# Kernel optimization log

Measured on AMD Instinct MI355X. Metric: run time of the kernel, lower is better.

The kernel has to match this reference:

```python
import jax, jax.numpy as jnp
import numpy as np

D = 512

def setup_inputs() -> dict:
    key = jax.random.key(0)
    k1, k2, k3, k4 = jax.random.split(key, 4)
    inputs = jax.random.normal(k1, (8, 2048, D), dtype=jnp.float32)
    # torch nn.Linear weights are [out, in]; y = x @ W.T
    Wk = jax.random.normal(k2, (D, D), dtype=jnp.float32) / np.sqrt(D)
    Wq = jax.random.normal(k3, (D, D), dtype=jnp.float32) / np.sqrt(D)
    Wv = jax.random.normal(k4, (D, D), dtype=jnp.float32) / np.sqrt(D)
    return {"inputs": inputs, "Wk": Wk, "Wq": Wq, "Wv": Wv}

def reference(inputs, Wk, Wq, Wv):
    # q/k/v: [B, S, D]
    q = jnp.einsum('bsd,ed->bse', inputs, Wq)
    k = jnp.einsum('bsd,ed->bse', inputs, Wk)
    v = jnp.einsum('bsd,ed->bse', inputs, Wv)
    scores = jnp.einsum('bqd,bkd->bqk', q, k) * 5.0  # note: scale is *5, not 1/sqrt(d)
    attn = jax.nn.softmax(scores, axis=-1)
    # dropout is identity in eval mode
    out = jnp.einsum('bqk,bkd->bqd', attn, v)
    return jnp.swapaxes(out, -2, -1)  # [B, D, S]
```

## Files before the change

kernel.cpp:

```cpp
#include <hip/hip_runtime.h>
#include <stdint.h>

typedef __attribute__((ext_vector_type(4))) float f32x4;
typedef __attribute__((ext_vector_type(8))) short short8;
typedef unsigned short u16;
typedef unsigned int u32;

#define DEV static __device__ __forceinline__

DEV u32 fbits(float f) { union { float f; u32 u; } v; v.f = f; return v.u; }
DEV float bits2f(u32 u) { union { u32 u; float f; } v; v.u = u; return v.f; }

DEV u16 f2bf_rne(float f) {
  u32 u = fbits(f);
  u32 r = u + 0x7fffu + ((u >> 16) & 1u);
  return (u16)(r >> 16);
}
DEV u16 f2bf_trunc(float f) { return (u16)(fbits(f) >> 16); }
DEV float bf2f(u16 h) { return bits2f(((u32)h) << 16); }

DEV void split2(float f, u16& h, u16& l) {
  h = f2bf_rne(f);
  float r = f - bf2f(h);
  l = f2bf_trunc(r);
}

DEV void gll16(const void* gsrc, char* ldsp) {
  __builtin_amdgcn_global_load_lds(
      (const __attribute__((address_space(1))) u32*)gsrc,
      (__attribute__((address_space(3))) u32*)ldsp,
      16, 0, 0);
}

DEV f32x4 mfma16(short8 a, short8 b, f32x4 c) {
  return __builtin_amdgcn_mfma_f32_16x16x32_bf16(a, b, c, 0, 0, 0);
}

template<int EPI>
__global__ __launch_bounds__(256, 1) void proj_gemm(
    const float* __restrict__ A, const float* __restrict__ Bm,
    u16* __restrict__ o0, u16* __restrict__ o1, float scale)
{
  extern __shared__ char smem[];
  const int tid = threadIdx.x;
  const int lane = tid & 63, wv = tid >> 6;
  const int wm = wv & 1, wn = wv >> 1;
  const int lm = lane & 15, lg = lane >> 4;
  const int n0 = blockIdx.x * 128, m0 = blockIdx.y * 128;

  f32x4 acc[4][4] = {};

  for (int k0 = 0; k0 < 512; k0 += 64) {
    __syncthreads();
    #pragma unroll
    for (int i = 0; i < 8; ++i) {
      int c = i * 256 + tid;
      int row = c >> 4, c4 = c & 15;
      f32x4 av = *(const f32x4*)(A + (size_t)(m0 + row) * 512 + (k0 + c4 * 4));
      f32x4 bv = *(const f32x4*)(Bm + (size_t)(n0 + row) * 512 + (k0 + c4 * 4));
      int base = row * 128 + ((((c4 >> 1) ^ (row & 7)) << 4) + (c4 & 1) * 8);
      u16 ah[4], al[4], bh[4], bl[4];
      #pragma unroll
      for (int j = 0; j < 4; ++j) { split2(av[j], ah[j], al[j]); split2(bv[j], bh[j], bl[j]); }
      *(ushort4*)(smem +         base) = make_ushort4(ah[0], ah[1], ah[2], ah[3]);
      *(ushort4*)(smem + 16384 + base) = make_ushort4(al[0], al[1], al[2], al[3]);
      *(ushort4*)(smem + 32768 + base) = make_ushort4(bh[0], bh[1], bh[2], bh[3]);
      *(ushort4*)(smem + 49152 + base) = make_ushort4(bl[0], bl[1], bl[2], bl[3]);
    }
    __syncthreads();
    #pragma unroll
    for (int ks = 0; ks < 2; ++ks) {
      short8 fah[4], fal[4], fbh[4], fbl[4];
      #pragma unroll
      for (int t = 0; t < 4; ++t) {
        int ar = wm * 64 + t * 16 + lm;
        int ac = (((ks * 4 + lg) ^ (ar & 7)) << 4);
        fah[t] = *(const short8*)(smem +         ar * 128 + ac);
        fal[t] = *(const short8*)(smem + 16384 + ar * 128 + ac);
        int br = wn * 64 + t * 16 + lm;
        int bc = (((ks * 4 + lg) ^ (br & 7)) << 4);
        fbh[t] = *(const short8*)(smem + 32768 + br * 128 + bc);
        fbl[t] = *(const short8*)(smem + 49152 + br * 128 + bc);
      }
      #pragma unroll
      for (int mt = 0; mt < 4; ++mt)
        #pragma unroll
        for (int nt = 0; nt < 4; ++nt) {
          acc[mt][nt] = mfma16(fah[mt], fbh[nt], acc[mt][nt]);
          acc[mt][nt] = mfma16(fah[mt], fbl[nt], acc[mt][nt]);
          acc[mt][nt] = mfma16(fal[mt], fbh[nt], acc[mt][nt]);
        }
    }
  }
  #pragma unroll
  for (int mt = 0; mt < 4; ++mt)
    #pragma unroll
    for (int nt = 0; nt < 4; ++nt)
      #pragma unroll
      for (int i = 0; i < 4; ++i) {
        float v = acc[mt][nt][i] * scale;
        int m = m0 + wm * 64 + mt * 16 + lg * 4 + i;
        int n = n0 + wn * 64 + nt * 16 + lm;
        if (EPI == 0) {
          u16 h, l; split2(v, h, l);
          o0[(size_t)m * 512 + n] = h;
          o1[(size_t)m * 512 + n] = l;
        } else {
          int r = n & 31;
          int cc = ((r >> 2) & 3) * 8 + ((r >> 4) << 2) + (r & 3);
          int n2 = (n & ~31) | cc;
          size_t addr = ((size_t)(n >> 11) << 20) | ((size_t)m << 11) | (size_t)(n2 & 2047);
          o0[addr] = f2bf_rne(v);
        }
      }
}

#define QH_OFF 0
#define QL_OFF 65536
#define STG0   131072
#define STG1   147456

DEV void stage_chunk(const u16* __restrict__ kh, const u16* __restrict__ kl,
                     const u16* __restrict__ vt, char* smem, int buf,
                     int b, int kt, int c, int tid) {
  char* dst = smem + (buf ? STG1 : STG0);
  if (c < 8) {
    const size_t kbase = (size_t)b * 2048 * 512 + (size_t)kt * 64 * 512 + c * 64;
    #pragma unroll
    for (int j = 0; j < 2; ++j) {
      int slot = j * 256 + tid;
      int r = slot >> 3, ch = slot & 7, sc = ch ^ (r & 7);
      size_t src = kbase + (size_t)r * 512 + sc * 8;
      gll16(kh + src, dst + slot * 16);
      gll16(kl + src, dst + 8192 + slot * 16);
    }
  } else {
    const int cv = c - 8;
    const size_t vbase = (size_t)b * 512 * 2048 + (size_t)(cv * 128) * 2048 + (size_t)kt * 64;
    #pragma unroll
    for (int j = 0; j < 4; ++j) {
      int slot = j * 256 + tid;
      int r = slot >> 3, ch = slot & 7, sc = ch ^ (r & 7);
      gll16(vt + vbase + (size_t)r * 2048 + sc * 8, dst + slot * 16);
    }
  }
}

__global__ __launch_bounds__(256, 1) void attn_fused(
    const u16* __restrict__ qh, const u16* __restrict__ ql,
    const u16* __restrict__ kh, const u16* __restrict__ kl,
    const u16* __restrict__ vt, float* __restrict__ out)
{
  extern __shared__ char smem[];
  const int tid = threadIdx.x;
  const int lane = tid & 63, wv = tid >> 6;
  const int lm = lane & 15, lg = lane >> 4;
  const int b = blockIdx.x, qt = blockIdx.y;

  {
    const size_t qbase = (size_t)(b * 2048 + qt * 64) * 512;
    #pragma unroll
    for (int it = 0; it < 16; ++it) {
      int slot = it * 256 + tid;
      int row = slot >> 6, ch = slot & 63;
      int sc = ch ^ (row & 7);
      size_t src = qbase + (size_t)row * 512 + sc * 8;
      gll16(qh + src, smem + QH_OFF + slot * 16);
      gll16(ql + src, smem + QL_OFF + slot * 16);
    }
  }
  stage_chunk(kh, kl, vt, smem, 0, b, 0, 0, tid);

  float m = -3e38f, l = 0.f;
  f32x4 oacc[32] = {};
  short8 pb0 = {}, pb1 = {};
  const int qrow = wv * 16 + lm;

  for (int kt = 0; kt < 32; ++kt) {
    f32x4 sacc[4] = {};
    #pragma unroll
    for (int c = 0; c < 12; ++c) {
      {
        int nk = kt, nc = c + 1;
        if (nc == 12) { nc = 0; nk = (kt + 1) & 31; }
        stage_chunk(kh, kl, vt, smem, (c + 1) & 1, b, nk, nc, tid);
      }
      if (c == 8) {
        float mx = fmaxf(fmaxf(fmaxf(sacc[0][0], sacc[0][1]), fmaxf(sacc[0][2], sacc[0][3])),
                         fmaxf(fmaxf(sacc[1][0], sacc[1][1]), fmaxf(sacc[1][2], sacc[1][3])));
        mx = fmaxf(mx, fmaxf(fmaxf(fmaxf(sacc[2][0], sacc[2][1]), fmaxf(sacc[2][2], sacc[2][3])),
                             fmaxf(fmaxf(sacc[3][0], sacc[3][1]), fmaxf(sacc[3][2], sacc[3][3]))));
        mx = fmaxf(mx, __shfl_xor(mx, 16, 64));
        mx = fmaxf(mx, __shfl_xor(mx, 32, 64));
        if (__any(mx > m)) {
          float mn = fmaxf(m, mx);
          float alpha = __expf(m - mn);
          m = mn;
          #pragma unroll
          for (int f = 0; f < 32; ++f) {
            oacc[f][0] *= alpha; oacc[f][1] *= alpha;
            oacc[f][2] *= alpha; oacc[f][3] *= alpha;
          }
          l *= alpha;
        }
        float sm = 0.f;
        #pragma unroll
        for (int t4 = 0; t4 < 4; ++t4)
          #pragma unroll
          for (int i = 0; i < 4; ++i) {
            float p = __expf(sacc[t4][i] - m);
            sacc[t4][i] = p;
            sm += p;
          }
        sm += __shfl_xor(sm, 16, 64);
        sm += __shfl_xor(sm, 32, 64);
        l += sm;
        #pragma unroll
        for (int j = 0; j < 4; ++j) {
          pb0[j]     = (short)f2bf_rne(sacc[0][j]);
          pb0[4 + j] = (short)f2bf_rne(sacc[1][j]);
          pb1[j]     = (short)f2bf_rne(sacc[2][j]);
          pb1[4 + j] = (short)f2bf_rne(sacc[3][j]);
        }
      }
      asm volatile("s_waitcnt vmcnt(4)" ::: "memory");
      __builtin_amdgcn_s_barrier();
      __builtin_amdgcn_sched_barrier(0);
      const char* bufp = smem + ((c & 1) ? STG1 : STG0);
      if (c < 8) {
        #pragma unroll
        for (int ks = 0; ks < 2; ++ks) {
          int qg = c * 8 + ks * 4 + lg;
          short8 bqh = *(const short8*)(smem + QH_OFF + qrow * 1024 + ((qg ^ (qrow & 7)) << 4));
          short8 bql = *(const short8*)(smem + QL_OFF + qrow * 1024 + ((qg ^ (qrow & 7)) << 4));
          #pragma unroll
          for (int t4 = 0; t4 < 4; ++t4) {
            int krow = t4 * 16 + lm;
            int kc = ((ks * 4 + lg) ^ (krow & 7)) << 4;
            short8 akh = *(const short8*)(bufp + krow * 128 + kc);
            short8 akl = *(const short8*)(bufp + 8192 + krow * 128 + kc);
            sacc[t4] = mfma16(akh, bqh, sacc[t4]);
            sacc[t4] = mfma16(akh, bql, sacc[t4]);
            sacc[t4] = mfma16(akl, bqh, sacc[t4]);
          }
        }
      } else {
        const int cv = c - 8;
        #pragma unroll
        for (int dt = 0; dt < 8; ++dt) {
          int vrow = dt * 16 + lm;
          short8 av0 = *(const short8*)(bufp + vrow * 128 + ((lg ^ (vrow & 7)) << 4));
          short8 av1 = *(const short8*)(bufp + vrow * 128 + (((4 + lg) ^ (vrow & 7)) << 4));
          f32x4 o = oacc[cv * 8 + dt];
          o = mfma16(av0, pb0, o);
          o = mfma16(av1, pb1, o);
          oacc[cv * 8 + dt] = o;
        }
      }
      __builtin_amdgcn_sched_barrier(0);
      __builtin_amdgcn_s_barrier();
    }
  }
  float linv = 1.0f / l;
  const int s = qt * 64 + wv * 16 + lm;
  float* ob = out + ((size_t)b << 20) + s;
  #pragma unroll
  for (int f = 0; f < 32; ++f)
    #pragma unroll
    for (int i = 0; i < 4; ++i) {
      int d = f * 16 + lg * 4 + i;
      ob[(size_t)d * 2048] = oacc[f][i] * linv;
    }
}

extern "C" void kernel_launch(void* const* d_in, const int* in_sizes, int n_in,
                              void* d_out, int out_size, void* d_ws, size_t ws_size,
                              hipStream_t stream) {
  (void)in_sizes; (void)n_in; (void)out_size; (void)ws_size;
  const float* x  = (const float*)d_in[0];
  const float* Wk = (const float*)d_in[1];
  const float* Wq = (const float*)d_in[2];
  const float* Wv = (const float*)d_in[3];
  float* out = (float*)d_out;

  const size_t SZ = (size_t)16384 * 512;
  u16* q_hi = (u16*)d_ws;
  u16* q_lo = q_hi + SZ;
  u16* k_hi = q_lo + SZ;
  u16* k_lo = k_hi + SZ;
  u16* v_t  = k_lo + SZ;

  (void)hipFuncSetAttribute(reinterpret_cast<const void*>(&proj_gemm<0>),
                            hipFuncAttributeMaxDynamicSharedMemorySize, 65536);
  (void)hipFuncSetAttribute(reinterpret_cast<const void*>(&proj_gemm<1>),
                            hipFuncAttributeMaxDynamicSharedMemorySize, 65536);
  (void)hipFuncSetAttribute(reinterpret_cast<const void*>(&attn_fused),
                            hipFuncAttributeMaxDynamicSharedMemorySize, 163840);

  dim3 blk(256);
  proj_gemm<0><<<dim3(4, 128), blk, 65536, stream>>>(x, Wq, q_hi, q_lo, 5.0f);
  proj_gemm<0><<<dim3(4, 128), blk, 65536, stream>>>(x, Wk, k_hi, k_lo, 1.0f);
  proj_gemm<1><<<dim3(128, 4), blk, 65536, stream>>>(Wv, x, v_t, nullptr, 1.0f);
  attn_fused<<<dim3(8, 32), blk, 163840, stream>>>(q_hi, q_lo, k_hi, k_lo, v_t, out);
}
```

Before: 337.0 us.

## Switch attention to fp16 split precision with fp8 residual term and restructured pipeline

Replaces the bf16 hi/lo three-MFMA score computation with fp16 hi/lo products for Q and an fp8 MFMA for the scaled K residual term. Q fragments are now read directly from global memory rather than staged in LDS. P is passed through LDS so that each wave owns a slice of the head dimension for PV, and the V projection moves to a single fp16 GEMM. The aim is fewer and cheaper MFMAs plus less LDS traffic, at the cost of more barriers, extra staging stages, and accuracy risk from fp16/fp8 rounding.

New measurement: 514.1 us. 52.5% more time.

```diff
diff --git a/kernel.cpp b/kernel.cpp
--- a/kernel.cpp
+++ b/kernel.cpp
@@ -1,10 +1,13 @@
 #include <hip/hip_runtime.h>
 #include <stdint.h>
+#include <math.h>
 
 typedef __attribute__((ext_vector_type(4))) float f32x4;
 typedef __attribute__((ext_vector_type(8))) short short8;
+typedef __attribute__((ext_vector_type(8))) _Float16 half8;
 typedef unsigned short u16;
 typedef unsigned int u32;
+typedef unsigned char u8;
 
 #define DEV static __device__ __forceinline__
 
@@ -18,11 +21,38 @@
 }
 DEV u16 f2bf_trunc(float f) { return (u16)(fbits(f) >> 16); }
 DEV float bf2f(u16 h) { return bits2f(((u32)h) << 16); }
-
 DEV void split2(float f, u16& h, u16& l) {
   h = f2bf_rne(f);
   float r = f - bf2f(h);
   l = f2bf_trunc(r);
+}
+
+DEV u16 f2h(float f) { union { _Float16 h; u16 u; } v; v.h = (_Float16)f; return v.u; }
+DEV float h2f(u16 u) { union { u16 u; _Float16 h; } v; v.u = u; return (float)v.h; }
+DEV half8 as_h8(short8 s) { union { short8 s; half8 h; } u; u.s = s; return u.h; }
+DEV uint2 pk4h(f32x4 v) {
+  uint2 w;
+  w.x = (u32)f2h(v[0]) | ((u32)f2h(v[1]) << 16);
+  w.y = (u32)f2h(v[2]) | ((u32)f2h(v[3]) << 16);
+  return w;
+}
+
+DEV u8 f32_to_e4m3(float f) {
+  u32 sb = (fbits(f) >> 24) & 0x80u;
+  float a = fabsf(f);
+  if (!(a >= 0.001953125f)) return (u8)sb;
+  if (a > 448.f) return (u8)(sb | 0x7e);
+  int e; float mant = frexpf(a, &e);
+  int E = e + 6;
+  if (E <= 0) {
+    int mi = (int)(a * 512.f + 0.5f);
+    if (mi > 7) return (u8)(sb | 0x08);
+    return (u8)(sb | mi);
+  }
+  int mi = (int)((mant * 2.f - 1.f) * 8.f + 0.5f);
+  if (mi == 8) { mi = 0; ++E; }
+  if (E > 15 || (E == 15 && mi > 6)) return (u8)(sb | 0x7e);
+  return (u8)(sb | (E << 3) | mi);
 }
 
 DEV void gll16(const void* gsrc, char* ldsp) {
@@ -35,11 +65,18 @@
 DEV f32x4 mfma16(short8 a, short8 b, f32x4 c) {
   return __builtin_amdgcn_mfma_f32_16x16x32_bf16(a, b, c, 0, 0, 0);
 }
-
-template<int EPI>
-__global__ __launch_bounds__(256, 1) void proj_gemm(
+DEV f32x4 mfmah(half8 a, half8 b, f32x4 c) {
+  return __builtin_amdgcn_mfma_f32_16x16x32_f16(a, b, c, 0, 0, 0);
+}
+DEV f32x4 mfma8(long a, long b, f32x4 c) {
+  return __builtin_amdgcn_mfma_f32_16x16x32_fp8_fp8(a, b, c, 0, 0, 0);
+}
+
+template<int MODE>
+__global__ __launch_bounds__(256, 1) void proj_qk(
     const float* __restrict__ A, const float* __restrict__ Bm,
-    u16* __restrict__ o0, u16* __restrict__ o1, float scale)
+    u16* __restrict__ o0, u16* __restrict__ o1, u8* __restrict__ o2,
+    float scale)
 {
   extern __shared__ char smem[];
   const int tid = threadIdx.x;
@@ -101,107 +138,195 @@
         float v = acc[mt][nt][i] * scale;
         int m = m0 + wm * 64 + mt * 16 + lg * 4 + i;
         int n = n0 + wn * 64 + nt * 16 + lm;
-        if (EPI == 0) {
-          u16 h, l; split2(v, h, l);
-          o0[(size_t)m * 512 + n] = h;
-          o1[(size_t)m * 512 + n] = l;
+        size_t idx = (size_t)m * 512 + n;
+        u16 h = f2h(v);
+        float res = v - h2f(h);
+        o0[idx] = h;
+        if (MODE == 0) {
+          o1[idx] = f2h(res);
+          o2[idx] = f32_to_e4m3(h2f(h));
         } else {
-          int r = n & 31;
-          int cc = ((r >> 2) & 3) * 8 + ((r >> 4) << 2) + (r & 3);
-          int n2 = (n & ~31) | cc;
-          size_t addr = ((size_t)(n >> 11) << 20) | ((size_t)m << 11) | (size_t)(n2 & 2047);
-          o0[addr] = f2bf_rne(v);
-        }
-      }
-}
-
-#define QH_OFF 0
-#define QL_OFF 65536
-#define STG0   131072
-#define STG1   147456
-
-DEV void stage_chunk(const u16* __restrict__ kh, const u16* __restrict__ kl,
-                     const u16* __restrict__ vt, char* smem, int buf,
-                     int b, int kt, int c, int tid) {
-  char* dst = smem + (buf ? STG1 : STG0);
-  if (c < 8) {
-    const size_t kbase = (size_t)b * 2048 * 512 + (size_t)kt * 64 * 512 + c * 64;
-    #pragma unroll
-    for (int j = 0; j < 2; ++j) {
-      int slot = j * 256 + tid;
-      int r = slot >> 3, ch = slot & 7, sc = ch ^ (r & 7);
-      size_t src = kbase + (size_t)r * 512 + sc * 8;
-      gll16(kh + src, dst + slot * 16);
-      gll16(kl + src, dst + 8192 + slot * 16);
-    }
-  } else {
-    const int cv = c - 8;
-    const size_t vbase = (size_t)b * 512 * 2048 + (size_t)(cv * 128) * 2048 + (size_t)kt * 64;
-    #pragma unroll
-    for (int j = 0; j < 4; ++j) {
-      int slot = j * 256 + tid;
-      int r = slot >> 3, ch = slot & 7, sc = ch ^ (r & 7);
-      gll16(vt + vbase + (size_t)r * 2048 + sc * 8, dst + slot * 16);
-    }
+          o2[idx] = f32_to_e4m3(res * 4096.f);
+        }
+      }
+}
+
+__global__ __launch_bounds__(256, 1) void proj_v(
+    const float* __restrict__ A, const float* __restrict__ Bm,
+    u16* __restrict__ o0)
+{
+  extern __shared__ char smem[];
+  const int tid = threadIdx.x;
+  const int lane = tid & 63, wv = tid >> 6;
+  const int wm = wv & 1, wn = wv >> 1;
+  const int lm = lane & 15, lg = lane >> 4;
+  const int n0 = blockIdx.x * 128, m0 = blockIdx.y * 128;
+
+  f32x4 acc[4][4] = {};
+
+  for (int k0 = 0; k0 < 512; k0 += 64) {
+    __syncthreads();
+    #pragma unroll
+    for (int i = 0; i < 8; ++i) {
+      int c = i * 256 + tid;
+      int row = c >> 4, c4 = c & 15;
+      f32x4 av = *(const f32x4*)(A + (size_t)(m0 + row) * 512 + (k0 + c4 * 4));
+      f32x4 bv = *(const f32x4*)(Bm + (size_t)(n0 + row) * 512 + (k0 + c4 * 4));
+      int base = row * 128 + ((c4 ^ (2 * (row & 7))) << 3);
+      *(uint2*)(smem +         base) = pk4h(av);
+      *(uint2*)(smem + 16384 + base) = pk4h(bv);
+    }
+    __syncthreads();
+    #pragma unroll
+    for (int ks = 0; ks < 2; ++ks) {
+      half8 fa[4], fb[4];
+      #pragma unroll
+      for (int t = 0; t < 4; ++t) {
+        int ar = wm * 64 + t * 16 + lm;
+        fa[t] = as_h8(*(const short8*)(smem + ar * 128 + (((ks * 4 + lg) ^ (ar & 7)) << 4)));
+        int br = wn * 64 + t * 16 + lm;
+        fb[t] = as_h8(*(const short8*)(smem + 16384 + br * 128 + (((ks * 4 + lg) ^ (br & 7)) << 4)));
+      }
+      #pragma unroll
+      for (int mt = 0; mt < 4; ++mt)
+        #pragma unroll
+        for (int nt = 0; nt < 4; ++nt)
+          acc[mt][nt] = mfmah(fa[mt], fb[nt], acc[mt][nt]);
+    }
+  }
+  #pragma unroll
+  for (int mt = 0; mt < 4; ++mt)
+    #pragma unroll
+    for (int nt = 0; nt < 4; ++nt)
+      #pragma unroll
+      for (int i = 0; i < 4; ++i) {
+        int m = m0 + wm * 64 + mt * 16 + lg * 4 + i;
+        int n = n0 + wn * 64 + nt * 16 + lm;
+        size_t addr = ((size_t)(n >> 11) << 20) | ((size_t)m << 11) | (size_t)(n & 2047);
+        o0[addr] = f2h(acc[mt][nt][i]);
+      }
+}
+
+#define KHB(i)  ((i) * 40960)
+#define KLB(i)  ((i) * 40960 + 32768)
+#define VBUF(i) (81920 + (i) * 16384)
+#define PB      114688
+#define AB      122880
+#define ALDS    123392
+
+DEV void stageK(const u16* __restrict__ khp, const u8* __restrict__ klp,
+                char* smem, int b, int kt, int c, int tid) {
+  char* dh = smem + KHB(c & 1);
+  char* dl = smem + KLB(c & 1);
+  const size_t rbase = (size_t)(b * 2048 + kt * 64);
+  #pragma unroll
+  for (int j = 0; j < 4; ++j) {
+    int slot = j * 256 + tid;
+    int r = slot >> 4, ch = slot & 15, sc = ch ^ (r & 7);
+    gll16(khp + (rbase + r) * 512 + c * 128 + sc * 8, dh + slot * 16);
+  }
+  #pragma unroll
+  for (int j = 0; j < 2; ++j) {
+    int slot = j * 256 + tid;
+    int r = slot >> 3, ch = slot & 7, sc = ch ^ (r & 7);
+    gll16(klp + (rbase + r) * 512 + c * 128 + sc * 16, dl + slot * 16);
+  }
+}
+DEV void stageV(const u16* __restrict__ vp, char* smem, int b, int kt, int cv, int tid) {
+  char* dst = smem + VBUF(cv & 1);
+  #pragma unroll
+  for (int j = 0; j < 4; ++j) {
+    int slot = j * 256 + tid;
+    int r = slot >> 3, ch = slot & 7, sc = ch ^ (r & 7);
+    gll16(vp + ((size_t)b << 20) + (size_t)(cv * 128 + r) * 2048 + kt * 64 + sc * 8,
+          dst + slot * 16);
   }
 }
 
 __global__ __launch_bounds__(256, 1) void attn_fused(
-    const u16* __restrict__ qh, const u16* __restrict__ ql,
-    const u16* __restrict__ kh, const u16* __restrict__ kl,
-    const u16* __restrict__ vt, float* __restrict__ out)
+    const u16* __restrict__ qh_g, const u16* __restrict__ ql_g,
+    const u8* __restrict__ q8_g, const u16* __restrict__ kh_g,
+    const u8* __restrict__ kl8_g, const u16* __restrict__ v_g,
+    float* __restrict__ out)
 {
   extern __shared__ char smem[];
   const int tid = threadIdx.x;
   const int lane = tid & 63, wv = tid >> 6;
   const int lm = lane & 15, lg = lane >> 4;
   const int b = blockIdx.x, qt = blockIdx.y;
-
-  {
-    const size_t qbase = (size_t)(b * 2048 + qt * 64) * 512;
-    #pragma unroll
-    for (int it = 0; it < 16; ++it) {
-      int slot = it * 256 + tid;
-      int row = slot >> 6, ch = slot & 63;
-      int sc = ch ^ (row & 7);
-      size_t src = qbase + (size_t)row * 512 + sc * 8;
-      gll16(qh + src, smem + QH_OFF + slot * 16);
-      gll16(ql + src, smem + QL_OFF + slot * 16);
-    }
-  }
-  stage_chunk(kh, kl, vt, smem, 0, b, 0, 0, tid);
+  const int srow = wv * 16 + lm;
+  const size_t qrow = (size_t)(b * 2048 + qt * 64 + srow);
+  const u16* qph = qh_g + qrow * 512;
+  const u16* qpl = ql_g + qrow * 512;
+  const u8*  qp8 = q8_g + qrow * 512;
+
+  stageK(kh_g, kl8_g, smem, b, 0, 0, tid);
+  __syncthreads();
 
   float m = -3e38f, l = 0.f;
-  f32x4 oacc[32] = {};
-  short8 pb0 = {}, pb1 = {};
-  const int qrow = wv * 16 + lm;
+  f32x4 oacc[4][2][4] = {};
 
   for (int kt = 0; kt < 32; ++kt) {
     f32x4 sacc[4] = {};
     #pragma unroll
-    for (int c = 0; c < 12; ++c) {
-      {
-        int nk = kt, nc = c + 1;
-        if (nc == 12) { nc = 0; nk = (kt + 1) & 31; }
-        stage_chunk(kh, kl, vt, smem, (c + 1) & 1, b, nk, nc, tid);
-      }
-      if (c == 8) {
+    for (int dc = 0; dc < 4; ++dc) {
+      if (dc < 3) stageK(kh_g, kl8_g, smem, b, kt, dc + 1, tid);
+      else        stageV(v_g, smem, b, kt, 0, tid);
+      __builtin_amdgcn_sched_barrier(0);
+      half8 qhf[4], qlf[4];
+      long  bq8[4];
+      #pragma unroll
+      for (int ks = 0; ks < 4; ++ks) {
+        int doff = dc * 128 + ks * 32 + lg * 8;
+        qhf[ks] = as_h8(*(const short8*)(qph + doff));
+        qlf[ks] = as_h8(*(const short8*)(qpl + doff));
+        bq8[ks] = *(const long*)(qp8 + doff);
+      }
+      const char* kb = smem + KHB(dc & 1);
+      const char* lb = smem + KLB(dc & 1);
+      __builtin_amdgcn_s_setprio(1);
+      #pragma unroll
+      for (int ks = 0; ks < 4; ++ks)
+        #pragma unroll
+        for (int t4 = 0; t4 < 4; ++t4) {
+          half8 akh = as_h8(*(const short8*)(
+              kb + (t4 * 16 + lm) * 256 + (((ks * 4 + lg) ^ (lm & 7)) << 4)));
+          sacc[t4] = mfmah(akh, qhf[ks], sacc[t4]);
+          sacc[t4] = mfmah(akh, qlf[ks], sacc[t4]);
+        }
+      f32x4 s3[4] = {};
+      #pragma unroll
+      for (int ks = 0; ks < 4; ++ks)
+        #pragma unroll
+        for (int t4 = 0; t4 < 4; ++t4) {
+          long akl = *(const long*)(
+              lb + (t4 * 16 + lm) * 128 +
+              ((((ks * 2 + (lg >> 1)) ^ (lm & 7)) << 4) + (lg & 1) * 8));
+          s3[t4] = mfma8(akl, bq8[ks], s3[t4]);
+        }
+      __builtin_amdgcn_s_setprio(0);
+      #pragma unroll
+      for (int t4 = 0; t4 < 4; ++t4) {
+        sacc[t4][0] += s3[t4][0] * 0.000244140625f;
+        sacc[t4][1] += s3[t4][1] * 0.000244140625f;
+        sacc[t4][2] += s3[t4][2] * 0.000244140625f;
+        sacc[t4][3] += s3[t4][3] * 0.000244140625f;
+      }
+      if (dc == 3) {
         float mx = fmaxf(fmaxf(fmaxf(sacc[0][0], sacc[0][1]), fmaxf(sacc[0][2], sacc[0][3])),
                          fmaxf(fmaxf(sacc[1][0], sacc[1][1]), fmaxf(sacc[1][2], sacc[1][3])));
         mx = fmaxf(mx, fmaxf(fmaxf(fmaxf(sacc[2][0], sacc[2][1]), fmaxf(sacc[2][2], sacc[2][3])),
                              fmaxf(fmaxf(sacc[3][0], sacc[3][1]), fmaxf(sacc[3][2], sacc[3][3]))));
         mx = fmaxf(mx, __shfl_xor(mx, 16, 64));
         mx = fmaxf(mx, __shfl_xor(mx, 32, 64));
+        float alpha;
         if (__any(mx > m)) {
           float mn = fmaxf(m, mx);
-          float alpha = __expf(m - mn);
+          alpha = __expf(m - mn);
           m = mn;
-          #pragma unroll
-          for (int f = 0; f < 32; ++f) {
-            oacc[f][0] *= alpha; oacc[f][1] *= alpha;
-            oacc[f][2] *= alpha; oacc[f][3] *= alpha;
-          }
           l *= alpha;
+        } else {
+          alpha = 1.0f;
         }
         float sm = 0.f;
         #pragma unroll
@@ -216,61 +341,75 @@
         sm += __shfl_xor(sm, 32, 64);
         l += sm;
         #pragma unroll
-        for (int j = 0; j < 4; ++j) {
-          pb0[j]     = (short)f2bf_rne(sacc[0][j]);
-          pb0[4 + j] = (short)f2bf_rne(sacc[1][j]);
-          pb1[j]     = (short)f2bf_rne(sacc[2][j]);
-          pb1[4 + j] = (short)f2bf_rne(sacc[3][j]);
-        }
-      }
-      asm volatile("s_waitcnt vmcnt(4)" ::: "memory");
-      __builtin_amdgcn_s_barrier();
+        for (int t4 = 0; t4 < 4; ++t4)
+          *(uint2*)(smem + PB + srow * 128 + (((4 * t4 + lg) ^ (2 * (srow & 7))) << 3))
+              = pk4h(sacc[t4]);
+        if (lg == 0) *(float*)(smem + AB + srow * 4) = alpha;
+      }
+      __syncthreads();
+    }
+    half8 pp[4][2];
+    #pragma unroll
+    for (int pc = 0; pc < 4; ++pc) {
+      if (pc < 3) stageV(v_g, smem, b, kt, pc + 1, tid);
+      else        stageK(kh_g, kl8_g, smem, b, (kt + 1) & 31, 0, tid);
       __builtin_amdgcn_sched_barrier(0);
-      const char* bufp = smem + ((c & 1) ? STG1 : STG0);
-      if (c < 8) {
+      if (pc == 0) {
+        float a4[4];
+        #pragma unroll
+        for (int st = 0; st < 4; ++st) {
+          a4[st] = *(const float*)(smem + AB + (st * 16 + lm) * 4);
+          #pragma unroll
+          for (int ks = 0; ks < 2; ++ks)
+            pp[st][ks] = as_h8(*(const short8*)(
+                smem + PB + (st * 16 + lm) * 128 + (((ks * 4 + lg) ^ (lm & 7)) << 4)));
+        }
+        #pragma unroll
+        for (int c2 = 0; c2 < 4; ++c2)
+          #pragma unroll
+          for (int dt = 0; dt < 2; ++dt)
+            #pragma unroll
+            for (int st = 0; st < 4; ++st) {
+              oacc[c2][dt][st][0] *= a4[st]; oacc[c2][dt][st][1] *= a4[st];
+              oacc[c2][dt][st][2] *= a4[st]; oacc[c2][dt][st][3] *= a4[st];
+            }
+      }
+      const char* vb = smem + VBUF(pc & 1);
+      __builtin_amdgcn_s_setprio(1);
+      #pragma unroll
+      for (int dt = 0; dt < 2; ++dt) {
+        int vrow = wv * 32 + dt * 16 + lm;
         #pragma unroll
         for (int ks = 0; ks < 2; ++ks) {
-          int qg = c * 8 + ks * 4 + lg;
-          short8 bqh = *(const short8*)(smem + QH_OFF + qrow * 1024 + ((qg ^ (qrow & 7)) << 4));
-          short8 bql = *(const short8*)(smem + QL_OFF + qrow * 1024 + ((qg ^ (qrow & 7)) << 4));
+          half8 av = as_h8(*(const short8*)(
+              vb + vrow * 128 + (((ks * 4 + lg) ^ (lm & 7)) << 4)));
           #pragma unroll
-          for (int t4 = 0; t4 < 4; ++t4) {
-            int krow = t4 * 16 + lm;
-            int kc = ((ks * 4 + lg) ^ (krow & 7)) << 4;
-            short8 akh = *(const short8*)(bufp + krow * 128 + kc);
-            short8 akl = *(const short8*)(bufp + 8192 + krow * 128 + kc);
-            sacc[t4] = mfma16(akh, bqh, sacc[t4]);
-            sacc[t4] = mfma16(akh, bql, sacc[t4]);
-            sacc[t4] = mfma16(akl, bqh, sacc[t4]);
-          }
-        }
-      } else {
-        const int cv = c - 8;
-        #pragma unroll
-        for (int dt = 0; dt < 8; ++dt) {
-          int vrow = dt * 16 + lm;
-          short8 av0 = *(const short8*)(bufp + vrow * 128 + ((lg ^ (vrow & 7)) << 4));
-          short8 av1 = *(const short8*)(bufp + vrow * 128 + (((4 + lg) ^ (vrow & 7)) << 4));
-          f32x4 o = oacc[cv * 8 + dt];
-          o = mfma16(av0, pb0, o);
-          o = mfma16(av1, pb1, o);
-          oacc[cv * 8 + dt] = o;
-        }
-      }
-      __builtin_amdgcn_sched_barrier(0);
-      __builtin_amdgcn_s_barrier();
-    }
-  }
-  float linv = 1.0f / l;
-  const int s = qt * 64 + wv * 16 + lm;
-  float* ob = out + ((size_t)b << 20) + s;
-  #pragma unroll
-  for (int f = 0; f < 32; ++f)
-    #pragma unroll
-    for (int i = 0; i < 4; ++i) {
-      int d = f * 16 + lg * 4 + i;
-      ob[(size_t)d * 2048] = oacc[f][i] * linv;
-    }
+          for (int st = 0; st < 4; ++st)
+            oacc[pc][dt][st] = mfmah(av, pp[st][ks], oacc[pc][dt][st]);
+        }
+      }
+      __builtin_amdgcn_s_setprio(0);
+      __syncthreads();
+    }
+  }
+  if (lg == 0) *(float*)(smem + AB + srow * 4) = l;
+  __syncthreads();
+  float li[4];
+  #pragma unroll
+  for (int st = 0; st < 4; ++st)
+    li[st] = 1.0f / *(const float*)(smem + AB + (st * 16 + lm) * 4);
+  float* ob = out + ((size_t)b << 20) + qt * 64;
+  #pragma unroll
+  for (int pc = 0; pc < 4; ++pc)
+    #pragma unroll
+    for (int dt = 0; dt < 2; ++dt)
+      #pragma unroll
+      for (int st = 0; st < 4; ++st)
+        #pragma unroll
+        for (int i = 0; i < 4; ++i) {
+          int d = pc * 128 + wv * 32 + dt * 16 + lg * 4 + i;
+          ob[(size_t)d * 2048 + st * 16 + lm] = oacc[pc][dt][st][i] * li[st];
+        }
 }
 
 extern "C" void kernel_launch(void* const* d_in, const int* in_sizes, int n_in,
@@ -284,22 +423,25 @@
   float* out = (float*)d_out;
 
   const size_t SZ = (size_t)16384 * 512;
-  u16* q_hi = (u16*)d_ws;
-  u16* q_lo = q_hi + SZ;
-  u16* k_hi = q_lo + SZ;
-  u16* k_lo = k_hi + SZ;
-  u16* v_t  = k_lo + SZ;
-
-  (void)hipFuncSetAttribute(reinterpret_cast<const void*>(&proj_gemm<0>),
+  u16* qh  = (u16*)d_ws;
+  u16* ql  = qh + SZ;
+  u16* kh  = ql + SZ;
+  u16* vt  = kh + SZ;
+  u8*  q8  = (u8*)(vt + SZ);
+  u8*  kl8 = q8 + SZ;
+
+  (void)hipFuncSetAttribute(reinterpret_cast<const void*>(&proj_qk<0>),
                             hipFuncAttributeMaxDynamicSharedMemorySize, 65536);
-  (void)hipFuncSetAttribute(reinterpret_cast<const void*>(&proj_gemm<1>),
+  (void)hipFuncSetAttribute(reinterpret_cast<const void*>(&proj_qk<2>),
                             hipFuncAttributeMaxDynamicSharedMemorySize, 65536);
+  (void)hipFuncSetAttribute(reinterpret_cast<const void*>(&proj_v),
+                            hipFuncAttributeMaxDynamicSharedMemorySize, 32768);
   (void)hipFuncSetAttribute(reinterpret_cast<const void*>(&attn_fused),
-                            hipFuncAttributeMaxDynamicSharedMemorySize, 163840);
+                            hipFuncAttributeMaxDynamicSharedMemorySize, ALDS);
 
   dim3 blk(256);
-  proj_gemm<0><<<dim3(4, 128), blk, 65536, stream>>>(x, Wq, q_hi, q_lo, 5.0f);
-  proj_gemm<0><<<dim3(4, 128), blk, 65536, stream>>>(x, Wk, k_hi, k_lo, 1.0f);
-  proj_gemm<1><<<dim3(128, 4), blk, 65536, stream>>>(Wv, x, v_t, nullptr, 1.0f);
-  attn_fused<<<dim3(8, 32), blk, 163840, stream>>>(q_hi, q_lo, k_hi, k_lo, v_t, out);
-}
+  proj_qk<0><<<dim3(4, 128), blk, 65536, stream>>>(x, Wq, qh, ql, q8, 5.0f);
+  proj_qk<2><<<dim3(4, 128), blk, 65536, stream>>>(x, Wk, kh, nullptr, kl8, 1.0f);
+  proj_v    <<<dim3(128, 4), blk, 32768, stream>>>(Wv, x, vt);
+  attn_fused<<<dim3(8, 32), blk, ALDS, stream>>>(qh, ql, q8, kh, kl8, vt, out);
+}
```
